# Kernel tuning notes

Hardware: AMD Instinct MI355X
Metric: run time of the kernel (lower is better)

The kernel has to match this reference:

```python
import math
import jax, jax.numpy as jnp
import numpy as np

D_MODEL = 768
N_HEADS = 12
HEAD_DIM = D_MODEL // N_HEADS
D_FF = 3072
LN_EPS = 1e-5


def _alibi_slopes(n_heads):
    def pow2(n):
        start = 2 ** (-(2 ** (-(math.log2(n) - 3))))
        return [start * start ** i for i in range(n)]
    if n_heads & (n_heads - 1) == 0:
        s = pow2(n_heads)
    else:
        c = 2 ** math.floor(math.log2(n_heads))
        s = pow2(c) + pow2(2 * c)[0::2][: n_heads - c]
    return np.asarray(s, dtype=np.float32)  # positive; negated at use site


def _ln(t, g, b):
    m = jnp.mean(t, axis=-1, keepdims=True)
    v = jnp.mean(jnp.square(t - m), axis=-1, keepdims=True)
    return (t - m) * jax.lax.rsqrt(v + LN_EPS) * g + b


def setup_inputs() -> dict:
    key = jax.random.key(0)
    ks = jax.random.split(key, 12)
    B, N = 4, 1025
    s = 0.02
    inp = {
        "x": jax.random.normal(ks[0], (B, N, D_MODEL), dtype=jnp.float32),
        "positions": jax.random.normal(ks[1], (B, N, 2), dtype=jnp.float32) * 8.0,
        "patch_sizes": jax.random.uniform(ks[2], (B,), dtype=jnp.float32, minval=0.5, maxval=2.0),
        "num_registers": 0,
        "ln1_g": jnp.ones((D_MODEL,), jnp.float32),
        "ln1_b": jnp.zeros((D_MODEL,), jnp.float32),
        "wq": jax.random.normal(ks[3], (D_MODEL, D_MODEL), jnp.float32) * s,
        "bq": jnp.zeros((D_MODEL,), jnp.float32),
        "wk": jax.random.normal(ks[4], (D_MODEL, D_MODEL), jnp.float32) * s,
        "bk": jnp.zeros((D_MODEL,), jnp.float32),
        "wv": jax.random.normal(ks[5], (D_MODEL, D_MODEL), jnp.float32) * s,
        "bv": jnp.zeros((D_MODEL,), jnp.float32),
        "wo": jax.random.normal(ks[6], (D_MODEL, D_MODEL), jnp.float32) * s,
        "bo": jnp.zeros((D_MODEL,), jnp.float32),
        "qn_g": jnp.ones((HEAD_DIM,), jnp.float32),
        "qn_b": jnp.zeros((HEAD_DIM,), jnp.float32),
        "kn_g": jnp.ones((HEAD_DIM,), jnp.float32),
        "kn_b": jnp.zeros((HEAD_DIM,), jnp.float32),
        "ln2_g": jnp.ones((D_MODEL,), jnp.float32),
        "ln2_b": jnp.zeros((D_MODEL,), jnp.float32),
        "w1": jax.random.normal(ks[7], (D_MODEL, D_FF), jnp.float32) * s,
        "b1": jnp.zeros((D_FF,), jnp.float32),
        "w2": jax.random.normal(ks[8], (D_FF, D_MODEL), jnp.float32) * s,
        "b2": jnp.zeros((D_MODEL,), jnp.float32),
    }
    return inp


def reference(x, positions, patch_sizes, num_registers,
              ln1_g, ln1_b, wq, bq, wk, bk, wv, bv, wo, bo,
              qn_g, qn_b, kn_g, kn_b, ln2_g, ln2_b, w1, b1, w2, b2):
    B, N, d = x.shape
    H, HD = N_HEADS, HEAD_DIM

    xn = _ln(x, ln1_g, ln1_b)
    q = (xn @ wq + bq).reshape(B, N, H, HD).transpose(0, 2, 1, 3)  # [B,H,N,HD]
    k = (xn @ wk + bk).reshape(B, N, H, HD).transpose(0, 2, 1, 3)
    v = (xn @ wv + bv).reshape(B, N, H, HD).transpose(0, 2, 1, 3)
    q = _ln(q, qn_g, qn_b)  # qk-norm over head_dim
    k = _ln(k, kn_g, kn_b)

    # 2-D ALiBi bias: [B,H,N,N]
    slopes = jnp.asarray(_alibi_slopes(H))  # positive
    ps = jnp.clip(patch_sizes, 1e-6)[:, None, None]
    diff = positions[:, :, None, :] - positions[:, None, :, :]  # [B,N,N,2]
    dist = jnp.sqrt(jnp.sum(jnp.square(diff), axis=-1)) / ps  # [B,N,N]
    bias = -slopes[None, :, None, None] * dist[:, None, :, :]
    idx = jnp.arange(N)
    special = (idx == 0) | ((idx >= 1) & (idx < 1 + num_registers))  # CLS + registers
    keep = (~special).astype(x.dtype)
    bias = bias * keep[None, None, :, None] * keep[None, None, None, :]

    scale = 1.0 / math.sqrt(HD)
    scores = jnp.einsum('bhqd,bhkd->bhqk', q, k) * scale + bias
    attn = jax.nn.softmax(scores, axis=-1)
    o = jnp.einsum('bhqk,bhkd->bhqd', attn, v)
    o = o.transpose(0, 2, 1, 3).reshape(B, N, d) @ wo + bo
    x = x + o

    xn2 = _ln(x, ln2_g, ln2_b)
    mlp = jax.nn.gelu(xn2 @ w1 + b1, approximate=False) @ w2 + b2
    return x + mlp
```

## Files before the change

kernel.cpp:

```cpp
#include <hip/hip_runtime.h>
#include <hip/hip_bf16.h>
#include <math.h>

typedef __attribute__((ext_vector_type(4))) float f32x4;
typedef __attribute__((ext_vector_type(8))) short short8;

#define DMODEL 768
#define NH 12
#define HD 64
#define DFF 3072
#define KVB 64
#define NSPLIT 3
#define QH 2
#define NP 1040

struct FalseC { static constexpr bool v = false; };
struct TrueC  { static constexpr bool v = true;  };

__device__ __forceinline__ short f2bf(float f) {
    union { float f; unsigned int u; } c; c.f = f;
    unsigned int r = c.u + 0x7FFFu + ((c.u >> 16) & 1u);
    return (short)(r >> 16);
}

__device__ __forceinline__ float bf2f(short s) {
    union { unsigned int u; float f; } c; c.u = ((unsigned int)(unsigned short)s) << 16;
    return c.f;
}

__device__ __forceinline__ void gload16(const void* g, void* l) {
    __builtin_amdgcn_global_load_lds((const __attribute__((address_space(1))) void*)g,
                                     (__attribute__((address_space(3))) void*)l, 16, 0, 0);
}

__device__ __forceinline__ int xcd_swz(int o, int nwg) {
    int q = nwg >> 3, r = nwg & 7, x = o & 7, i = o >> 3;
    return (x < r ? x * (q + 1) : r * (q + 1) + (x - r) * q) + i;
}

__global__ __launch_bounds__(256) void transpose_all(
        const float* __restrict__ wq, const float* __restrict__ wk, const float* __restrict__ wv,
        const float* __restrict__ wo, const float* __restrict__ w1, const float* __restrict__ w2,
        short* __restrict__ wt_qkv, short* __restrict__ wt_o,
        short* __restrict__ wt_1, short* __restrict__ wt_2) {
    __shared__ float tile[32][33];
    int bid = blockIdx.x;
    const float* src; short* dst; int K, Nn, nx;
    if (bid < 2304) {
        int s = bid / 576; bid -= s * 576;
        src = (s == 0) ? wq : (s == 1) ? wk : (s == 2) ? wv : wo;
        dst = (s < 3) ? (wt_qkv + (size_t)s * 768 * 768) : wt_o;
        K = 768; Nn = 768; nx = 24;
    } else if (bid < 4608) {
        bid -= 2304; src = w1; dst = wt_1; K = 768; Nn = 3072; nx = 96;
    } else {
        bid -= 4608; src = w2; dst = wt_2; K = 3072; Nn = 768; nx = 24;
    }
    const int n0 = (bid % nx) * 32, k0 = (bid / nx) * 32;
    const int tx = threadIdx.x & 31, ty = threadIdx.x >> 5;
    #pragma unroll
    for (int i = ty; i < 32; i += 8) {
        int k = k0 + i, n = n0 + tx;
        tile[i][tx] = (k < K && n < Nn) ? src[(size_t)k * Nn + n] : 0.f;
    }
    __syncthreads();
    #pragma unroll
    for (int i = ty; i < 32; i += 8) {
        int n = n0 + i, k = k0 + tx;
        if (n < Nn && k < K) dst[(size_t)n * K + k] = f2bf(tile[tx][i]);
    }
}

__global__ void concat_bias(const float* __restrict__ bq, const float* __restrict__ bk,
                            const float* __restrict__ bv, float* __restrict__ out) {
    int i = blockIdx.x * 256 + threadIdx.x;
    if (i < 2304) out[i] = (i < 768) ? bq[i] : (i < 1536 ? bk[i - 768] : bv[i - 1536]);
}

__global__ __launch_bounds__(256) void ln_rows(const float* __restrict__ x, const float* __restrict__ g,
                                               const float* __restrict__ bb, short* __restrict__ out, int M) {
    __shared__ float red[8];
    const int row = blockIdx.x;
    const int tid = threadIdx.x;
    const float* xr = x + (size_t)row * DMODEL;
    float v[3];
    #pragma unroll
    for (int j = 0; j < 3; j++) v[j] = xr[tid + j * 256];
    float s = v[0] + v[1] + v[2];
    #pragma unroll
    for (int mk = 32; mk; mk >>= 1) s += __shfl_xor(s, mk);
    if ((tid & 63) == 0) red[tid >> 6] = s;
    __syncthreads();
    const float mean = (red[0] + red[1] + red[2] + red[3]) * (1.0f / 768.0f);
    float sq = 0.f;
    #pragma unroll
    for (int j = 0; j < 3; j++) { float d = v[j] - mean; sq += d * d; }
    #pragma unroll
    for (int mk = 32; mk; mk >>= 1) sq += __shfl_xor(sq, mk);
    if ((tid & 63) == 0) red[4 + (tid >> 6)] = sq;
    __syncthreads();
    const float var = (red[4] + red[5] + red[6] + red[7]) * (1.0f / 768.0f);
    const float rstd = rsqrtf(var + 1e-5f);
    short* orow = out + (size_t)row * DMODEL;
    #pragma unroll
    for (int j = 0; j < 3; j++) {
        int col = tid + j * 256;
        orow[col] = f2bf((v[j] - mean) * rstd * g[col] + bb[col]);
    }
}

__global__ __launch_bounds__(256) void gemm_qkv(const short* __restrict__ A, const short* __restrict__ Bt,
        const float* __restrict__ bias,
        const float* __restrict__ qg, const float* __restrict__ qb2,
        const float* __restrict__ kg, const float* __restrict__ kb2,
        short* __restrict__ Qb, short* __restrict__ Kb, short* __restrict__ Vtp,
        int M, int B, int Nseq) {
    __shared__ short As[64 * 64];
    __shared__ short Bs[128 * 64];
    const int nbx = 18, nby = (M + 63) / 64;
    const int sid = xcd_swz(blockIdx.x, nbx * nby);
    const int n0 = (sid % nbx) * 128, m0 = (sid / nbx) * 64;
    const int tid = threadIdx.x, w = tid >> 6, lane = tid & 63, g = lane >> 4, cl = lane & 15;
    const int wm = w >> 1, wn = w & 1;
    f32x4 acc[2][4];
    #pragma unroll
    for (int a = 0; a < 2; a++)
        #pragma unroll
        for (int b2 = 0; b2 < 4; b2++) acc[a][b2] = (f32x4){0.f, 0.f, 0.f, 0.f};
    for (int kk = 0; kk < 768; kk += 64) {
        #pragma unroll
        for (int c = 0; c < 1536; c += 256) {
            int ci = c + tid;
            if (ci < 512) {
                int row = ci >> 3, p = ci & 7;
                int arow = m0 + row; if (arow >= M) arow = M - 1;
                gload16(A + (size_t)arow * 768 + kk + ((p ^ (row & 7)) << 3), &As[ci * 8]);
            } else {
                int c2 = ci - 512;
                int row = c2 >> 3, p = c2 & 7;
                gload16(Bt + (size_t)(n0 + row) * 768 + kk + ((p ^ (row & 7)) << 3), &Bs[c2 * 8]);
            }
        }
        __syncthreads();
        #pragma unroll
        for (int kh = 0; kh < 2; ++kh) {
            short8 af[2], bf[4];
            #pragma unroll
            for (int mi = 0; mi < 2; mi++) {
                int ra = wm * 32 + mi * 16 + cl;
                af[mi] = *(const short8*)&As[ra * 64 + ((((kh << 2) + g) ^ (ra & 7)) << 3)];
            }
            #pragma unroll
            for (int ni = 0; ni < 4; ni++) {
                int rb = wn * 64 + ni * 16 + cl;
                bf[ni] = *(const short8*)&Bs[rb * 64 + ((((kh << 2) + g) ^ (rb & 7)) << 3)];
            }
            #pragma unroll
            for (int mi = 0; mi < 2; mi++)
                #pragma unroll
                for (int ni = 0; ni < 4; ni++)
                    acc[mi][ni] = __builtin_amdgcn_mfma_f32_16x16x32_bf16(af[mi], bf[ni], acc[mi][ni], 0, 0, 0);
        }
        __syncthreads();
    }
    const int t = n0 / 768;
    const int h = (n0 - t * 768) / 64 + wn;
    const int b0 = m0 / Nseq, bnd = (b0 + 1) * Nseq;
    float bi[4];
    #pragma unroll
    for (int ni = 0; ni < 4; ni++) bi[ni] = bias[n0 + wn * 64 + ni * 16 + cl];
    if (t < 2) {
        const float* gp = (t == 0) ? qg : kg;
        const float* bp = (t == 0) ? qb2 : kb2;
        float gv[4], bv[4];
        #pragma unroll
        for (int ni = 0; ni < 4; ni++) { gv[ni] = gp[ni * 16 + cl]; bv[ni] = bp[ni * 16 + cl]; }
        short* out = (t == 0) ? Qb : Kb;
        #pragma unroll
        for (int mi = 0; mi < 2; mi++)
            #pragma unroll
            for (int r = 0; r < 4; r++) {
                int row = m0 + wm * 32 + mi * 16 + 4 * g + r;
                float v0 = acc[mi][0][r] + bi[0];
                float v1 = acc[mi][1][r] + bi[1];
                float v2 = acc[mi][2][r] + bi[2];
                float v3 = acc[mi][3][r] + bi[3];
                float sx = v0 + v1 + v2 + v3;
                float sxx = v0 * v0 + v1 * v1 + v2 * v2 + v3 * v3;
                #pragma unroll
                for (int mk = 8; mk; mk >>= 1) { sx += __shfl_xor(sx, mk); sxx += __shfl_xor(sxx, mk); }
                float mean = sx * (1.0f / 64.0f);
                float var = sxx * (1.0f / 64.0f) - mean * mean;
                float rstd = rsqrtf(var + 1e-5f);
                if (row < M) {
                    int bb = (row >= bnd) ? b0 + 1 : b0;
                    int n = row - bb * Nseq;
                    size_t base = (((size_t)bb * NH + h) * Nseq + n) * HD + cl;
                    out[base + 0]  = f2bf(fmaf((v0 - mean) * rstd, gv[0], bv[0]));
                    out[base + 16] = f2bf(fmaf((v1 - mean) * rstd, gv[1], bv[1]));
                    out[base + 32] = f2bf(fmaf((v2 - mean) * rstd, gv[2], bv[2]));
                    out[base + 48] = f2bf(fmaf((v3 - mean) * rstd, gv[3], bv[3]));
                }
            }
    } else {
        #pragma unroll
        for (int mi = 0; mi < 2; mi++)
            #pragma unroll
            for (int r = 0; r < 4; r++) {
                int row = m0 + wm * 32 + mi * 16 + 4 * g + r;
                if (row < M) {
                    int bb = (row >= bnd) ? b0 + 1 : b0;
                    int n = row - bb * Nseq;
                    size_t vb2 = ((size_t)bb * NH + h) * HD + cl;
                    #pragma unroll
                    for (int ni = 0; ni < 4; ni++)
                        Vtp[(vb2 + ni * 16) * NP + n] = f2bf(acc[mi][ni][r] + bi[ni]);
                }
            }
    }
}

template<int EPI, int BM, int BN>
__global__ __launch_bounds__(256) void gemm_bt(const short* __restrict__ A, const short* __restrict__ Bt,
        const float* __restrict__ bias, const float* __restrict__ res, void* __restrict__ Cv,
        int M, int Nn, int K) {
    constexpr int RM = BM / 32, RN = BN / 32;
    __shared__ short As[BM * 64];
    __shared__ short Bs[BN * 64];
    const int nbx = Nn / BN, nby = (M + BM - 1) / BM;
    const int sid = xcd_swz(blockIdx.x, nbx * nby);
    const int n0 = (sid % nbx) * BN, m0 = (sid / nbx) * BM;
    const int tid = threadIdx.x, w = tid >> 6, lane = tid & 63, g = lane >> 4, cl = lane & 15;
    const int wm = w >> 1, wn = w & 1;
    f32x4 acc[RM][RN];
    #pragma unroll
    for (int a = 0; a < RM; a++)
        #pragma unroll
        for (int b2 = 0; b2 < RN; b2++) acc[a][b2] = (f32x4){0.f, 0.f, 0.f, 0.f};
    constexpr int CHA = BM * 8, CHT = (BM + BN) * 8;
    for (int kk = 0; kk < K; kk += 64) {
        #pragma unroll
        for (int c = 0; c < CHT; c += 256) {
            int ci = c + tid;
            if (ci < CHA) {
                int row = ci >> 3, p = ci & 7;
                int arow = m0 + row; if (arow >= M) arow = M - 1;
                gload16(A + (size_t)arow * K + kk + ((p ^ (row & 7)) << 3), &As[ci * 8]);
            } else {
                int c2 = ci - CHA;
                int row = c2 >> 3, p = c2 & 7;
                gload16(Bt + (size_t)(n0 + row) * K + kk + ((p ^ (row & 7)) << 3), &Bs[c2 * 8]);
            }
        }
        __syncthreads();
        #pragma unroll
        for (int kh = 0; kh < 2; ++kh) {
            short8 af[RM], bf[RN];
            #pragma unroll
            for (int mi = 0; mi < RM; mi++) {
                int ra = wm * (BM / 2) + mi * 16 + cl;
                af[mi] = *(const short8*)&As[ra * 64 + ((((kh << 2) + g) ^ (ra & 7)) << 3)];
            }
            #pragma unroll
            for (int ni = 0; ni < RN; ni++) {
                int rb = wn * (BN / 2) + ni * 16 + cl;
                bf[ni] = *(const short8*)&Bs[rb * 64 + ((((kh << 2) + g) ^ (rb & 7)) << 3)];
            }
            #pragma unroll
            for (int mi = 0; mi < RM; mi++)
                #pragma unroll
                for (int ni = 0; ni < RN; ni++)
                    acc[mi][ni] = __builtin_amdgcn_mfma_f32_16x16x32_bf16(af[mi], bf[ni], acc[mi][ni], 0, 0, 0);
        }
        __syncthreads();
    }
    #pragma unroll
    for (int ni = 0; ni < RN; ++ni) {
        int col = n0 + wn * (BN / 2) + ni * 16 + cl;
        float bi = bias[col];
        #pragma unroll
        for (int mi = 0; mi < RM; ++mi) {
            int rb = m0 + wm * (BM / 2) + mi * 16 + 4 * g;
            #pragma unroll
            for (int r = 0; r < 4; ++r) {
                int row = rb + r;
                if (row < M) {
                    float vv = acc[mi][ni][r] + bi;
                    if (EPI == 1) {
                        vv += res[(size_t)row * Nn + col];
                        ((float*)Cv)[(size_t)row * Nn + col] = vv;
                    } else {
                        float ge = 0.5f * vv * (1.0f + erff(vv * 0.70710678118654752f));
                        ((short*)Cv)[(size_t)row * Nn + col] = f2bf(ge);
                    }
                }
            }
        }
    }
}

__global__ __launch_bounds__(256, 3) void attn_kernel(
        const short* __restrict__ Qb, const short* __restrict__ Kb, const short* __restrict__ Vt,
        const float* __restrict__ pos, const float* __restrict__ psz, const int* __restrict__ nregp,
        short* __restrict__ opart, float* __restrict__ ppart, int B, int Nn, int nwg) {
    __shared__ short Vbuf[2][QH][4096];
    __shared__ short Pl[4][QH][16][68];
    __shared__ float Rs[4][QH][16];
    const int nqt = (Nn + 63) >> 6;
    const int sid = xcd_swz(blockIdx.x, nwg);
    const int qt = sid % nqt;
    const int rem = sid / nqt;
    const int nyy = (NH / QH) * NSPLIT;
    const int yy = rem % nyy;
    const int b = rem / nyy;
    const int h0 = (yy / NSPLIT) * QH, sp = yy % NSPLIT;
    const int tid = threadIdx.x, w = tid >> 6, lane = tid & 63, g = lane >> 4, cl = lane & 15;
    const int nreg1 = 1 + nregp[0];
    const float inv_ps = 1.0f / fmaxf(psz[b], 1e-6f);
    const float sc2 = 0.125f * 1.4426950408889634f;
    const size_t bq = (size_t)b * Nn;
    const float2* __restrict__ pos2 = (const float2*)pos;
    const int q0 = qt * 64 + w * 16;

    size_t bh[QH], vb[QH];
    short8 qa[QH][2];
    float sP[QH];
    int qr = q0 + cl; if (qr > Nn - 1) qr = Nn - 1;
    const float2 qp = pos2[bq + qr];
    const float keepq = (qr < nreg1) ? 0.f : 1.f;
    #pragma unroll
    for (int hh = 0; hh < QH; hh++) {
        int h = h0 + hh;
        bh[hh] = ((size_t)b * NH + h) * (size_t)Nn;
        vb[hh] = ((size_t)b * NH + h) * (size_t)(HD * NP);
        float slope = (h < 8) ? exp2f(-(float)(h + 1)) : exp2f(-0.5f - (float)(h - 8));
        sP[hh] = slope * inv_ps * 1.4426950408889634f * keepq;
        const short* qptr = Qb + (bh[hh] + qr) * HD;
        qa[hh][0] = *(const short8*)(qptr + 8 * g);
        qa[hh][1] = *(const short8*)(qptr + 32 + 8 * g);
    }

    int qi[4];
    #pragma unroll
    for (int i = 0; i < 4; i++) qi[i] = q0 + 4 * g + i;

    f32x4 o[QH][4];
    float psum[QH] = {0.f, 0.f};
    #pragma unroll
    for (int hh = 0; hh < QH; hh++)
        #pragma unroll
        for (int c2 = 0; c2 < 4; c2++) o[hh][c2] = (f32x4){0.f, 0.f, 0.f, 0.f};

    const int ktiles = (Nn + KVB - 1) / KVB;
    const int tps = (ktiles + NSPLIT - 1) / NSPLIT;
    const int t0 = sp * tps, t1 = min(ktiles, t0 + tps);

    auto stage = [&](int buf, int kt) {
        const int kv0 = kt * KVB;
        #pragma unroll
        for (int it = 0; it < 2 * QH; ++it) {
            int idx = it * 256 + tid;
            int hh = idx >> 9, rm = idx & 511;
            int d = rm >> 3, slot = rm & 7;
            int kvs = kv0 + ((slot ^ (d & 7)) << 3);
            gload16(Vt + vb[hh] + (size_t)d * NP + kvs, &Vbuf[buf][hh][rm * 8]);
        }
    };

    stage(0, t0);
    int cur = 0;
    for (int kt = t0; kt < t1; ++kt) {
        const int kv0 = kt * KVB;
        __syncthreads();
        if (kt + 1 < t1) stage(cur ^ 1, kt + 1);

        auto qbody = [&](int qt2, auto mc, auto tc) {
            constexpr bool KMASK = decltype(mc)::v;
            constexpr bool TAIL  = decltype(tc)::v;
            const int kbase = kv0 + qt2 * 16;
            int krow = kbase + cl;
            if (TAIL) krow = min(krow, Nn - 1);
            const short* kp0 = Kb + (bh[0] + krow) * HD;
            const short* kp1 = Kb + (bh[1] + krow) * HD;
            const short8 k00 = *(const short8*)(kp0 + 8 * g);
            const short8 k01 = *(const short8*)(kp0 + 32 + 8 * g);
            const short8 k10 = *(const short8*)(kp1 + 8 * g);
            const short8 k11 = *(const short8*)(kp1 + 32 + 8 * g);
            f32x4 s0 = __builtin_amdgcn_mfma_f32_16x16x32_bf16(k00, qa[0][0], (f32x4){0.f,0.f,0.f,0.f}, 0, 0, 0);
            s0 = __builtin_amdgcn_mfma_f32_16x16x32_bf16(k01, qa[0][1], s0, 0, 0, 0);
            f32x4 s1 = __builtin_amdgcn_mfma_f32_16x16x32_bf16(k10, qa[1][0], (f32x4){0.f,0.f,0.f,0.f}, 0, 0, 0);
            s1 = __builtin_amdgcn_mfma_f32_16x16x32_bf16(k11, qa[1][1], s1, 0, 0, 0);
            const int kb4 = kbase + 4 * g;
            float p0v[4], p1v[4];
            #pragma unroll
            for (int i = 0; i < 4; i++) {
                int ki = kb4 + i;
                int kic = TAIL ? min(ki, Nn - 1) : ki;
                float2 kp2 = pos2[bq + kic];
                float dx = qp.x - kp2.x, dy = qp.y - kp2.y;
                float dist = sqrtf(fmaf(dx, dx, dy * dy));
                if (KMASK) dist *= (ki < nreg1) ? 0.f : 1.f;
                float e0 = fmaf(s0[i], sc2, -12.0f);
                e0 = fmaf(-sP[0], dist, e0);
                float p0 = exp2f(e0);
                float e1 = fmaf(s1[i], sc2, -12.0f);
                e1 = fmaf(-sP[1], dist, e1);
                float p1 = exp2f(e1);
                if (TAIL) { bool vl = ki < Nn; p0 = vl ? p0 : 0.f; p1 = vl ? p1 : 0.f; }
                psum[0] += p0; psum[1] += p1;
                p0v[i] = p0; p1v[i] = p1;
            }
            unsigned int w00, w01, w10, w11;
            asm("v_cvt_pk_bf16_f32 %0, %1, %2" : "=v"(w00) : "v"(p0v[0]), "v"(p0v[1]));
            asm("v_cvt_pk_bf16_f32 %0, %1, %2" : "=v"(w01) : "v"(p0v[2]), "v"(p0v[3]));
            asm("v_cvt_pk_bf16_f32 %0, %1, %2" : "=v"(w10) : "v"(p1v[0]), "v"(p1v[1]));
            asm("v_cvt_pk_bf16_f32 %0, %1, %2" : "=v"(w11) : "v"(p1v[2]), "v"(p1v[3]));
            *(unsigned int*)&Pl[w][0][cl][qt2 * 16 + 4 * g]     = w00;
            *(unsigned int*)&Pl[w][0][cl][qt2 * 16 + 4 * g + 2] = w01;
            *(unsigned int*)&Pl[w][1][cl][qt2 * 16 + 4 * g]     = w10;
            *(unsigned int*)&Pl[w][1][cl][qt2 * 16 + 4 * g + 2] = w11;
        };

        const bool istail = (kv0 + KVB > Nn);
        if (!istail) {
            if (kv0 < nreg1) {
                qbody(0, TrueC{}, FalseC{}); qbody(1, TrueC{}, FalseC{});
                qbody(2, TrueC{}, FalseC{}); qbody(3, TrueC{}, FalseC{});
            } else {
                qbody(0, FalseC{}, FalseC{}); qbody(1, FalseC{}, FalseC{});
                qbody(2, FalseC{}, FalseC{}); qbody(3, FalseC{}, FalseC{});
            }
        } else {
            qbody(0, FalseC{}, TrueC{}); qbody(1, FalseC{}, TrueC{});
            qbody(2, FalseC{}, TrueC{}); qbody(3, FalseC{}, TrueC{});
        }

        __builtin_amdgcn_s_setprio(1);
        #pragma unroll
        for (int hh = 0; hh < QH; hh++) {
            #pragma unroll
            for (int ks = 0; ks < 2; ++ks) {
                const short8 pf = *(const short8*)&Pl[w][hh][cl][ks * 32 + 8 * g];
                #pragma unroll
                for (int c2 = 0; c2 < 4; c2++) {
                    const int d = c2 * 16 + cl;
                    const int slot = ((ks << 2) + g) ^ (cl & 7);
                    const short8 vf = *(const short8*)&Vbuf[cur][hh][d * 64 + slot * 8];
                    o[hh][c2] = __builtin_amdgcn_mfma_f32_16x16x32_bf16(pf, vf, o[hh][c2], 0, 0, 0);
                }
            }
        }
        __builtin_amdgcn_s_setprio(0);
        cur ^= 1;
    }

    #pragma unroll
    for (int hh = 0; hh < QH; hh++) {
        float r = psum[hh];
        r += __shfl_xor(r, 16);
        r += __shfl_xor(r, 32);
        if (lane < 16) Rs[w][hh][lane] = r;
    }
    float4 rs0 = *(const float4*)&Rs[w][0][4 * g];
    float4 rs1 = *(const float4*)&Rs[w][1][4 * g];
    #pragma unroll
    for (int i = 0; i < 4; i++) {
        if (qi[i] < Nn) {
            #pragma unroll
            for (int hh = 0; hh < QH; hh++) {
                size_t rbase = (((size_t)sp * B + b) * NH + (h0 + hh)) * Nn + qi[i];
                #pragma unroll
                for (int c2 = 0; c2 < 4; c2++)
                    opart[rbase * HD + c2 * 16 + cl] = f2bf(o[hh][c2][i]);
                if (cl == 0) ppart[rbase] = hh ? rs1[i] : rs0[i];
            }
        }
    }
}

__global__ __launch_bounds__(256) void attn_reduce(const short* __restrict__ opart,
        const float* __restrict__ ppart, short* __restrict__ Ob, int B, int Nn) {
    const int rows = B * NH * Nn;
    const int row = blockIdx.x * 4 + (threadIdx.x >> 6);
    if (row >= rows) return;
    const int d = threadIdx.x & 63;
    const int n = row % Nn;
    const int bh = row / Nn;
    const int h = bh % NH, b = bh / NH;
    const size_t stride = (size_t)B * NH * Nn;
    float o = 0.f, p = 0.f;
    #pragma unroll
    for (int s = 0; s < NSPLIT; s++) {
        o += bf2f(opart[((size_t)s * stride + row) * HD + d]);
        p += ppart[(size_t)s * stride + row];
    }
    Ob[((size_t)b * Nn + n) * DMODEL + h * HD + d] = f2bf(o / p);
}

extern "C" void kernel_launch(void* const* d_in, const int* in_sizes, int n_in,
                              void* d_out, int out_size, void* d_ws, size_t ws_size,
                              hipStream_t stream) {
    const float* x    = (const float*)d_in[0];
    const float* pos  = (const float*)d_in[1];
    const float* psz  = (const float*)d_in[2];
    const int*   nreg = (const int*)d_in[3];
    const float* ln1g = (const float*)d_in[4];
    const float* ln1b = (const float*)d_in[5];
    const float* wq   = (const float*)d_in[6];
    const float* bq   = (const float*)d_in[7];
    const float* wk   = (const float*)d_in[8];
    const float* bk   = (const float*)d_in[9];
    const float* wv   = (const float*)d_in[10];
    const float* bv   = (const float*)d_in[11];
    const float* wo   = (const float*)d_in[12];
    const float* bo   = (const float*)d_in[13];
    const float* qng  = (const float*)d_in[14];
    const float* qnb  = (const float*)d_in[15];
    const float* kng  = (const float*)d_in[16];
    const float* knb  = (const float*)d_in[17];
    const float* ln2g = (const float*)d_in[18];
    const float* ln2b = (const float*)d_in[19];
    const float* w1   = (const float*)d_in[20];
    const float* b1   = (const float*)d_in[21];
    const float* w2   = (const float*)d_in[22];
    const float* b2   = (const float*)d_in[23];

    const int B  = in_sizes[2];
    const int Nn = in_sizes[1] / (2 * B);
    const int M  = B * Nn;

    char* ws = (char*)d_ws;
    size_t off = 0;
    auto alloc = [&](size_t bytes) -> char* {
        char* p = ws + off;
        off += (bytes + 255) & ~(size_t)255;
        return p;
    };
    short* wt_qkv   = (short*)alloc((size_t)2304 * 768 * 2);
    short* wt_o     = (short*)alloc((size_t)768 * 768 * 2);
    short* wt_1     = (short*)alloc((size_t)3072 * 768 * 2);
    short* wt_2     = (short*)alloc((size_t)768 * 3072 * 2);
    float* bias_qkv = (float*)alloc(2304 * 4);
    short* xn       = (short*)alloc((size_t)M * 768 * 2);
    short* Qb       = (short*)alloc((size_t)M * 768 * 2);
    short* Kb       = (short*)alloc((size_t)M * 768 * 2);
    short* Vt       = (short*)alloc((size_t)B * NH * HD * NP * 2 + 4096);
    short* Ob       = (short*)alloc((size_t)M * 768 * 2);
    float* x1       = (float*)alloc((size_t)M * 768 * 4);
    short* xn2      = (short*)alloc((size_t)M * 768 * 2);
    short* hmid     = (short*)alloc((size_t)M * 3072 * 2);
    float* ppart    = (float*)alloc((size_t)NSPLIT * B * NH * Nn * 4);
    short* opart    = hmid;

    dim3 blk(256);
    transpose_all<<<6912, blk, 0, stream>>>(wq, wk, wv, wo, w1, w2, wt_qkv, wt_o, wt_1, wt_2);
    concat_bias<<<9, blk, 0, stream>>>(bq, bk, bv, bias_qkv);

    const int MB64 = (M + 63) / 64;
    ln_rows<<<M, blk, 0, stream>>>(x, ln1g, ln1b, xn, M);
    gemm_qkv<<<18 * MB64, blk, 0, stream>>>(xn, wt_qkv, bias_qkv, qng, qnb, kng, knb,
                                            Qb, Kb, Vt, M, B, Nn);
    const int nqt = (Nn + 63) / 64;
    const int anwg = nqt * (NH / QH) * NSPLIT * B;
    attn_kernel<<<anwg, blk, 0, stream>>>(Qb, Kb, Vt, pos, psz, nreg, opart, ppart, B, Nn, anwg);
    attn_reduce<<<(B * NH * Nn + 3) / 4, blk, 0, stream>>>(opart, ppart, Ob, B, Nn);
    gemm_bt<1, 64, 64><<<12 * MB64, blk, 0, stream>>>(Ob, wt_o, bo, x, x1, M, 768, 768);
    ln_rows<<<M, blk, 0, stream>>>(x1, ln2g, ln2b, xn2, M);
    gemm_bt<2, 64, 128><<<24 * MB64, blk, 0, stream>>>(xn2, wt_1, b1, nullptr, hmid, M, 3072, 768);
    gemm_bt<1, 64, 64><<<12 * MB64, blk, 0, stream>>>(hmid, wt_2, b2, x1, (float*)d_out, M, 768, 3072);
}
```

Before: 249.9 us.

## Redistribute P fragments via lane shuffles instead of LDS, reduce KV split

The attention kernel now converts the softmax probabilities into the MFMA A-operand layout with cross-lane shuffles in registers, dropping the per-wave LDS P buffer and its write/read round trip. The PV MFMAs are interleaved per 32-key half with the QK/exp work. It also reduces the KV split count from 3 to 2 and raises the launch-bounds occupancy hint from 3 to 4 blocks. This removes LDS traffic and frees shared memory, at the cost of extra shuffle instructions, tighter register limits and fewer parallel work groups with longer per-group loops.

Result: slower. 261.1 us (+4.5%).

```diff
diff --git a/kernel.cpp b/kernel.cpp
--- a/kernel.cpp
+++ b/kernel.cpp
@@ -10,7 +10,7 @@
 #define HD 64
 #define DFF 3072
 #define KVB 64
-#define NSPLIT 3
+#define NSPLIT 2
 #define QH 2
 #define NP 1040
 
@@ -299,12 +299,11 @@
     }
 }
 
-__global__ __launch_bounds__(256, 3) void attn_kernel(
+__global__ __launch_bounds__(256, 4) void attn_kernel(
         const short* __restrict__ Qb, const short* __restrict__ Kb, const short* __restrict__ Vt,
         const float* __restrict__ pos, const float* __restrict__ psz, const int* __restrict__ nregp,
         short* __restrict__ opart, float* __restrict__ ppart, int B, int Nn, int nwg) {
     __shared__ short Vbuf[2][QH][4096];
-    __shared__ short Pl[4][QH][16][68];
     __shared__ float Rs[4][QH][16];
     const int nqt = (Nn + 63) >> 6;
     const int sid = xcd_swz(blockIdx.x, nwg);
@@ -367,6 +366,17 @@
         }
     };
 
+    auto redist = [&](unsigned A, unsigned Bv, unsigned& vLo, unsigned& vHi) {
+        unsigned As32 = (unsigned)__shfl_xor((int)A, 32);
+        unsigned Bs32 = (unsigned)__shfl_xor((int)Bv, 32);
+        unsigned d0 = (lane < 32) ? A : Bs32;
+        unsigned d1 = (lane < 32) ? As32 : Bv;
+        unsigned d1x = (unsigned)__shfl_xor((int)d1, 16);
+        unsigned d0x = (unsigned)__shfl_xor((int)d0, 16);
+        vLo = (lane & 16) ? d1x : d0;
+        vHi = (lane & 16) ? d1 : d0x;
+    };
+
     stage(0, t0);
     int cur = 0;
     for (int kt = t0; kt < t1; ++kt) {
@@ -374,7 +384,7 @@
         __syncthreads();
         if (kt + 1 < t1) stage(cur ^ 1, kt + 1);
 
-        auto qbody = [&](int qt2, auto mc, auto tc) {
+        auto qbody = [&](int qt2, unsigned (&outp)[2][2], auto mc, auto tc) {
             constexpr bool KMASK = decltype(mc)::v;
             constexpr bool TAIL  = decltype(tc)::v;
             const int kbase = kv0 + qt2 * 16;
@@ -410,47 +420,38 @@
                 psum[0] += p0; psum[1] += p1;
                 p0v[i] = p0; p1v[i] = p1;
             }
-            unsigned int w00, w01, w10, w11;
-            asm("v_cvt_pk_bf16_f32 %0, %1, %2" : "=v"(w00) : "v"(p0v[0]), "v"(p0v[1]));
-            asm("v_cvt_pk_bf16_f32 %0, %1, %2" : "=v"(w01) : "v"(p0v[2]), "v"(p0v[3]));
-            asm("v_cvt_pk_bf16_f32 %0, %1, %2" : "=v"(w10) : "v"(p1v[0]), "v"(p1v[1]));
-            asm("v_cvt_pk_bf16_f32 %0, %1, %2" : "=v"(w11) : "v"(p1v[2]), "v"(p1v[3]));
-            *(unsigned int*)&Pl[w][0][cl][qt2 * 16 + 4 * g]     = w00;
-            *(unsigned int*)&Pl[w][0][cl][qt2 * 16 + 4 * g + 2] = w01;
-            *(unsigned int*)&Pl[w][1][cl][qt2 * 16 + 4 * g]     = w10;
-            *(unsigned int*)&Pl[w][1][cl][qt2 * 16 + 4 * g + 2] = w11;
+            asm("v_cvt_pk_bf16_f32 %0, %1, %2" : "=v"(outp[0][0]) : "v"(p0v[0]), "v"(p0v[1]));
+            asm("v_cvt_pk_bf16_f32 %0, %1, %2" : "=v"(outp[0][1]) : "v"(p0v[2]), "v"(p0v[3]));
+            asm("v_cvt_pk_bf16_f32 %0, %1, %2" : "=v"(outp[1][0]) : "v"(p1v[0]), "v"(p1v[1]));
+            asm("v_cvt_pk_bf16_f32 %0, %1, %2" : "=v"(outp[1][1]) : "v"(p1v[2]), "v"(p1v[3]));
         };
 
         const bool istail = (kv0 + KVB > Nn);
-        if (!istail) {
-            if (kv0 < nreg1) {
-                qbody(0, TrueC{}, FalseC{}); qbody(1, TrueC{}, FalseC{});
-                qbody(2, TrueC{}, FalseC{}); qbody(3, TrueC{}, FalseC{});
+        #pragma unroll
+        for (int ks = 0; ks < 2; ++ks) {
+            unsigned pa[2][2], pb[2][2];
+            if (!istail) {
+                if (kv0 < nreg1) { qbody(2 * ks, pa, TrueC{}, FalseC{});  qbody(2 * ks + 1, pb, TrueC{}, FalseC{}); }
+                else             { qbody(2 * ks, pa, FalseC{}, FalseC{}); qbody(2 * ks + 1, pb, FalseC{}, FalseC{}); }
             } else {
-                qbody(0, FalseC{}, FalseC{}); qbody(1, FalseC{}, FalseC{});
-                qbody(2, FalseC{}, FalseC{}); qbody(3, FalseC{}, FalseC{});
-            }
-        } else {
-            qbody(0, FalseC{}, TrueC{}); qbody(1, FalseC{}, TrueC{});
-            qbody(2, FalseC{}, TrueC{}); qbody(3, FalseC{}, TrueC{});
-        }
-
-        __builtin_amdgcn_s_setprio(1);
-        #pragma unroll
-        for (int hh = 0; hh < QH; hh++) {
-            #pragma unroll
-            for (int ks = 0; ks < 2; ++ks) {
-                const short8 pf = *(const short8*)&Pl[w][hh][cl][ks * 32 + 8 * g];
+                qbody(2 * ks, pa, FalseC{}, TrueC{}); qbody(2 * ks + 1, pb, FalseC{}, TrueC{});
+            }
+            __builtin_amdgcn_s_setprio(1);
+            #pragma unroll
+            for (int hh = 0; hh < QH; hh++) {
+                union { unsigned u[4]; short8 s; } pu;
+                redist(pa[hh][0], pb[hh][0], pu.u[0], pu.u[2]);
+                redist(pa[hh][1], pb[hh][1], pu.u[1], pu.u[3]);
                 #pragma unroll
                 for (int c2 = 0; c2 < 4; c2++) {
                     const int d = c2 * 16 + cl;
                     const int slot = ((ks << 2) + g) ^ (cl & 7);
                     const short8 vf = *(const short8*)&Vbuf[cur][hh][d * 64 + slot * 8];
-                    o[hh][c2] = __builtin_amdgcn_mfma_f32_16x16x32_bf16(pf, vf, o[hh][c2], 0, 0, 0);
+                    o[hh][c2] = __builtin_amdgcn_mfma_f32_16x16x32_bf16(pu.s, vf, o[hh][c2], 0, 0, 0);
                 }
             }
-        }
-        __builtin_amdgcn_s_setprio(0);
+            __builtin_amdgcn_s_setprio(0);
+        }
         cur ^= 1;
     }
 
```

## Precompute ALiBi distance matrix in separate kernel and load it in attention

Applied to the files above, without the earlier changes.

Adds a kernel that materializes the per-batch q-k distance matrix (pre-scaled by patch size, log2e and the key mask) into a padded fp32 buffer. The attention kernel then loads a float4 of distances per fragment instead of gathering key positions and computing sqrt per element, and drops the special-key masking branch. This trades per-head-pair recomputation of sqrt and position gathers for an extra launch plus about 17 MB of global memory writes and reads.

After: 257.4 us. 3.0% more time.

```diff
diff --git a/kernel.cpp b/kernel.cpp
--- a/kernel.cpp
+++ b/kernel.cpp
@@ -13,6 +13,7 @@
 #define NSPLIT 3
 #define QH 2
 #define NP 1040
+#define NP2 1028
 
 struct FalseC { static constexpr bool v = false; };
 struct TrueC  { static constexpr bool v = true;  };
@@ -75,6 +76,23 @@
                             const float* __restrict__ bv, float* __restrict__ out) {
     int i = blockIdx.x * 256 + threadIdx.x;
     if (i < 2304) out[i] = (i < 768) ? bq[i] : (i < 1536 ? bk[i - 768] : bv[i - 1536]);
+}
+
+__global__ __launch_bounds__(256) void dist_kernel(const float* __restrict__ pos,
+        const float* __restrict__ psz, const int* __restrict__ nregp,
+        float* __restrict__ distm, int Nn) {
+    const int k = blockIdx.x * 256 + threadIdx.x;
+    const int q = blockIdx.y, b = blockIdx.z;
+    if (k >= Nn) return;
+    const int nreg1 = 1 + nregp[0];
+    const float2* __restrict__ pos2 = (const float2*)pos;
+    const float2 qp = pos2[(size_t)b * Nn + q];
+    const float2 kp = pos2[(size_t)b * Nn + k];
+    const float dx = qp.x - kp.x, dy = qp.y - kp.y;
+    const float keepk = (k < nreg1) ? 0.f : 1.f;
+    const float inv_ps = 1.0f / fmaxf(psz[b], 1e-6f);
+    distm[((size_t)b * Nn + q) * NP2 + k] =
+        sqrtf(fmaf(dx, dx, dy * dy)) * keepk * inv_ps * 1.4426950408889634f;
 }
 
 __global__ __launch_bounds__(256) void ln_rows(const float* __restrict__ x, const float* __restrict__ g,
@@ -301,7 +319,7 @@
 
 __global__ __launch_bounds__(256, 3) void attn_kernel(
         const short* __restrict__ Qb, const short* __restrict__ Kb, const short* __restrict__ Vt,
-        const float* __restrict__ pos, const float* __restrict__ psz, const int* __restrict__ nregp,
+        const float* __restrict__ distm, const int* __restrict__ nregp,
         short* __restrict__ opart, float* __restrict__ ppart, int B, int Nn, int nwg) {
     __shared__ short Vbuf[2][QH][4096];
     __shared__ short Pl[4][QH][16][68];
@@ -316,25 +334,22 @@
     const int h0 = (yy / NSPLIT) * QH, sp = yy % NSPLIT;
     const int tid = threadIdx.x, w = tid >> 6, lane = tid & 63, g = lane >> 4, cl = lane & 15;
     const int nreg1 = 1 + nregp[0];
-    const float inv_ps = 1.0f / fmaxf(psz[b], 1e-6f);
     const float sc2 = 0.125f * 1.4426950408889634f;
-    const size_t bq = (size_t)b * Nn;
-    const float2* __restrict__ pos2 = (const float2*)pos;
     const int q0 = qt * 64 + w * 16;
 
     size_t bh[QH], vb[QH];
     short8 qa[QH][2];
     float sP[QH];
     int qr = q0 + cl; if (qr > Nn - 1) qr = Nn - 1;
-    const float2 qp = pos2[bq + qr];
     const float keepq = (qr < nreg1) ? 0.f : 1.f;
+    const float* __restrict__ drow = distm + ((size_t)b * Nn + qr) * NP2;
     #pragma unroll
     for (int hh = 0; hh < QH; hh++) {
         int h = h0 + hh;
         bh[hh] = ((size_t)b * NH + h) * (size_t)Nn;
         vb[hh] = ((size_t)b * NH + h) * (size_t)(HD * NP);
         float slope = (h < 8) ? exp2f(-(float)(h + 1)) : exp2f(-0.5f - (float)(h - 8));
-        sP[hh] = slope * inv_ps * 1.4426950408889634f * keepq;
+        sP[hh] = slope * keepq;
         const short* qptr = Qb + (bh[hh] + qr) * HD;
         qa[hh][0] = *(const short8*)(qptr + 8 * g);
         qa[hh][1] = *(const short8*)(qptr + 32 + 8 * g);
@@ -374,9 +389,8 @@
         __syncthreads();
         if (kt + 1 < t1) stage(cur ^ 1, kt + 1);
 
-        auto qbody = [&](int qt2, auto mc, auto tc) {
-            constexpr bool KMASK = decltype(mc)::v;
-            constexpr bool TAIL  = decltype(tc)::v;
+        auto qbody = [&](int qt2, auto tc) {
+            constexpr bool TAIL = decltype(tc)::v;
             const int kbase = kv0 + qt2 * 16;
             int krow = kbase + cl;
             if (TAIL) krow = min(krow, Nn - 1);
@@ -386,6 +400,7 @@
             const short8 k01 = *(const short8*)(kp0 + 32 + 8 * g);
             const short8 k10 = *(const short8*)(kp1 + 8 * g);
             const short8 k11 = *(const short8*)(kp1 + 32 + 8 * g);
+            const f32x4 dv = *(const f32x4*)(drow + kbase + 4 * g);
             f32x4 s0 = __builtin_amdgcn_mfma_f32_16x16x32_bf16(k00, qa[0][0], (f32x4){0.f,0.f,0.f,0.f}, 0, 0, 0);
             s0 = __builtin_amdgcn_mfma_f32_16x16x32_bf16(k01, qa[0][1], s0, 0, 0, 0);
             f32x4 s1 = __builtin_amdgcn_mfma_f32_16x16x32_bf16(k10, qa[1][0], (f32x4){0.f,0.f,0.f,0.f}, 0, 0, 0);
@@ -394,19 +409,13 @@
             float p0v[4], p1v[4];
             #pragma unroll
             for (int i = 0; i < 4; i++) {
-                int ki = kb4 + i;
-                int kic = TAIL ? min(ki, Nn - 1) : ki;
-                float2 kp2 = pos2[bq + kic];
-                float dx = qp.x - kp2.x, dy = qp.y - kp2.y;
-                float dist = sqrtf(fmaf(dx, dx, dy * dy));
-                if (KMASK) dist *= (ki < nreg1) ? 0.f : 1.f;
                 float e0 = fmaf(s0[i], sc2, -12.0f);
-                e0 = fmaf(-sP[0], dist, e0);
+                e0 = fmaf(-sP[0], dv[i], e0);
                 float p0 = exp2f(e0);
                 float e1 = fmaf(s1[i], sc2, -12.0f);
-                e1 = fmaf(-sP[1], dist, e1);
+                e1 = fmaf(-sP[1], dv[i], e1);
                 float p1 = exp2f(e1);
-                if (TAIL) { bool vl = ki < Nn; p0 = vl ? p0 : 0.f; p1 = vl ? p1 : 0.f; }
+                if (TAIL) { bool vl = (kb4 + i) < Nn; p0 = vl ? p0 : 0.f; p1 = vl ? p1 : 0.f; }
                 psum[0] += p0; psum[1] += p1;
                 p0v[i] = p0; p1v[i] = p1;
             }
@@ -423,16 +432,11 @@
 
         const bool istail = (kv0 + KVB > Nn);
         if (!istail) {
-            if (kv0 < nreg1) {
-                qbody(0, TrueC{}, FalseC{}); qbody(1, TrueC{}, FalseC{});
-                qbody(2, TrueC{}, FalseC{}); qbody(3, TrueC{}, FalseC{});
-            } else {
-                qbody(0, FalseC{}, FalseC{}); qbody(1, FalseC{}, FalseC{});
-                qbody(2, FalseC{}, FalseC{}); qbody(3, FalseC{}, FalseC{});
-            }
+            qbody(0, FalseC{}); qbody(1, FalseC{});
+            qbody(2, FalseC{}); qbody(3, FalseC{});
         } else {
-            qbody(0, FalseC{}, TrueC{}); qbody(1, FalseC{}, TrueC{});
-            qbody(2, FalseC{}, TrueC{}); qbody(3, FalseC{}, TrueC{});
+            qbody(0, TrueC{}); qbody(1, TrueC{});
+            qbody(2, TrueC{}); qbody(3, TrueC{});
         }
 
         __builtin_amdgcn_s_setprio(1);
@@ -550,11 +554,13 @@
     short* xn2      = (short*)alloc((size_t)M * 768 * 2);
     short* hmid     = (short*)alloc((size_t)M * 3072 * 2);
     float* ppart    = (float*)alloc((size_t)NSPLIT * B * NH * Nn * 4);
+    float* distm    = (float*)alloc((size_t)B * Nn * NP2 * 4);
     short* opart    = hmid;
 
     dim3 blk(256);
     transpose_all<<<6912, blk, 0, stream>>>(wq, wk, wv, wo, w1, w2, wt_qkv, wt_o, wt_1, wt_2);
     concat_bias<<<9, blk, 0, stream>>>(bq, bk, bv, bias_qkv);
+    dist_kernel<<<dim3((Nn + 255) / 256, Nn, B), blk, 0, stream>>>(pos, psz, nreg, distm, Nn);
 
     const int MB64 = (M + 63) / 64;
     ln_rows<<<M, blk, 0, stream>>>(x, ln1g, ln1b, xn, M);
@@ -562,7 +568,7 @@
                                             Qb, Kb, Vt, M, B, Nn);
     const int nqt = (Nn + 63) / 64;
     const int anwg = nqt * (NH / QH) * NSPLIT * B;
-    attn_kernel<<<anwg, blk, 0, stream>>>(Qb, Kb, Vt, pos, psz, nreg, opart, ppart, B, Nn, anwg);
+    attn_kernel<<<anwg, blk, 0, stream>>>(Qb, Kb, Vt, distm, nreg, opart, ppart, B, Nn, anwg);
     attn_reduce<<<(B * NH * Nn + 3) / 4, blk, 0, stream>>>(opart, ppart, Ob, B, Nn);
     gemm_bt<1, 64, 64><<<12 * MB64, blk, 0, stream>>>(Ob, wt_o, bo, x, x1, M, 768, 768);
     ln_rows<<<M, blk, 0, stream>>>(x1, ln2g, ln2b, xn2, M);
```
